# Kernel tuning notes

Measured on AMD Instinct MI355X. Metric: run time of the kernel, lower is better.

Reference implementation:

```python
import jax, jax.numpy as jnp
import numpy as np
from jax import lax

K = 7          # neighborhood kernel size
NUM_HEADS = 4
EPS = 1e-5


def layernorm(x, w, b):
    mu = x.mean(-1, keepdims=True)
    var = ((x - mu) ** 2).mean(-1, keepdims=True)
    return (x - mu) * lax.rsqrt(var + EPS) * w + b


def window_idx(n, k):
    # NATTEN border behavior: window is shifted (not shrunk) at edges.
    start = jnp.clip(jnp.arange(n) - k // 2, 0, n - k)
    return start[:, None] + jnp.arange(k)  # [n, k]


def neighborhood_attention(x, qkv_w, qkv_b, rpb, proj_w, proj_b):
    B, H, W, C = x.shape
    nh, k = NUM_HEADS, K
    hd = C // nh
    scale = hd ** -0.5
    qkv = (x @ qkv_w + qkv_b).reshape(B, H, W, 3, nh, hd)
    q = jnp.transpose(qkv[:, :, :, 0], (0, 3, 1, 2, 4)) * scale  # [B,nh,H,W,hd]
    kk = jnp.transpose(qkv[:, :, :, 1], (0, 3, 1, 2, 4))
    vv = jnp.transpose(qkv[:, :, :, 2], (0, 3, 1, 2, 4))

    ri = window_idx(H, k)  # [H,k]
    ci = window_idx(W, k)  # [W,k]

    def gather(t):  # [B,nh,H,W,hd] -> [B,nh,H,W,k,k,hd]
        t = t[:, :, ri]           # [B,nh,H,k,W,hd]
        t = t[:, :, :, :, ci]     # [B,nh,H,k,W,k,hd]
        return jnp.transpose(t, (0, 1, 2, 4, 3, 5, 6))

    k_nb = gather(kk)
    v_nb = gather(vv).reshape(B, nh, H, W, k * k, hd)

    attn = jnp.einsum('bnhwd,bnhwijd->bnhwij', q, k_nb)  # [B,nh,H,W,k,k]

    # relative positional bias, rpb: [nh, 2k-1, 2k-1]
    br = ri - jnp.arange(H)[:, None] + (k - 1)  # [H,k] in [0, 2k-2]
    bc = ci - jnp.arange(W)[:, None] + (k - 1)  # [W,k]
    bias = rpb[:, br]                 # [nh,H,k,2k-1]
    bias = bias[:, :, :, bc]          # [nh,H,k,W,k]
    bias = jnp.transpose(bias, (0, 1, 3, 2, 4))  # [nh,H,W,k,k]

    attn = jax.nn.softmax((attn + bias[None]).reshape(B, nh, H, W, k * k), axis=-1)
    out = jnp.einsum('bnhwl,bnhwld->bnhwd', attn, v_nb)
    out = jnp.transpose(out, (0, 2, 3, 1, 4)).reshape(B, H, W, C)
    return out @ proj_w + proj_b


def mlp(x, w1, b1, w2, b2):
    return jax.nn.gelu(x @ w1 + b1, approximate=False) @ w2 + b2


def nat_block_forward(x, norm1_w, norm1_b, qkv_w, qkv_b, rpb, proj_w, proj_b,
                      norm2_w, norm2_b, fc1_w, fc1_b, fc2_w, fc2_b,
                      conv_w, dnorm_w, dnorm_b):
    depth = norm1_w.shape[0]
    for i in range(depth):
        h = layernorm(x, norm1_w[i], norm1_b[i])
        h = neighborhood_attention(h, qkv_w[i], qkv_b[i], rpb[i], proj_w[i], proj_b[i])
        x = x + h
        x = x + mlp(layernorm(x, norm2_w[i], norm2_b[i]),
                    fc1_w[i], fc1_b[i], fc2_w[i], fc2_b[i])
    # ConvDownsampler: 3x3 stride-2 conv (no bias) + LayerNorm, channels-last
    y = lax.conv_general_dilated(x, conv_w, (2, 2), ((1, 1), (1, 1)),
                                 dimension_numbers=('NHWC', 'HWIO', 'NHWC'))
    y = layernorm(y, dnorm_w, dnorm_b)
    return (y, x)


def setup_inputs() -> dict:
    key = jax.random.key(0)
    ks = jax.random.split(key, 12)
    B, H, W, C = 2, 56, 56, 128
    depth, nh, k = 2, NUM_HEADS, K
    hidden = 4 * C
    init = lambda kk, shape: jax.random.normal(kk, shape, jnp.float32) * 0.02
    return {
        'x': jax.random.normal(ks[0], (B, H, W, C), jnp.float32),
        'norm1_w': jnp.ones((depth, C), jnp.float32),
        'norm1_b': jnp.zeros((depth, C), jnp.float32),
        'qkv_w': init(ks[1], (depth, C, 3 * C)),
        'qkv_b': jnp.zeros((depth, 3 * C), jnp.float32),
        'rpb': init(ks[2], (depth, nh, 2 * k - 1, 2 * k - 1)),
        'proj_w': init(ks[3], (depth, C, C)),
        'proj_b': jnp.zeros((depth, C), jnp.float32),
        'norm2_w': jnp.ones((depth, C), jnp.float32),
        'norm2_b': jnp.zeros((depth, C), jnp.float32),
        'fc1_w': init(ks[4], (depth, C, hidden)),
        'fc1_b': jnp.zeros((depth, hidden), jnp.float32),
        'fc2_w': init(ks[5], (depth, hidden, C)),
        'fc2_b': jnp.zeros((depth, C), jnp.float32),
        'conv_w': init(ks[6], (3, 3, C, 2 * C)),
        'dnorm_w': jnp.ones((2 * C,), jnp.float32),
        'dnorm_b': jnp.zeros((2 * C,), jnp.float32),
    }


def reference(x, norm1_w, norm1_b, qkv_w, qkv_b, rpb, proj_w, proj_b,
              norm2_w, norm2_b, fc1_w, fc1_b, fc2_w, fc2_b,
              conv_w, dnorm_w, dnorm_b):
    return nat_block_forward(x, norm1_w, norm1_b, qkv_w, qkv_b, rpb, proj_w,
                             proj_b, norm2_w, norm2_b, fc1_w, fc1_b, fc2_w,
                             fc2_b, conv_w, dnorm_w, dnorm_b)
```

## Files before the change

### kernel.cpp

```cpp
#include <hip/hip_runtime.h>
#include <stdint.h>


typedef __attribute__((ext_vector_type(8))) short bf16x8;
typedef __attribute__((ext_vector_type(4))) float f32x4;

__device__ __forceinline__ float bf2f(uint16_t u) {
  union { uint32_t u; float f; } t;
  t.u = (uint32_t)u << 16;
  return t.f;
}
__device__ __forceinline__ uint16_t f2bf(float f) {
  union { float f; uint32_t u; } t;
  t.f = f;
  return (uint16_t)((t.u + 0x7FFFu + ((t.u >> 16) & 1u)) >> 16);
}

struct PrepArgs {
  const float* src[9];
  uint16_t* dst[9];
  int K[9], N[9];
  int cum[10];
};

__global__ __launch_bounds__(256) void prep_weights(PrepArgs a) {
  __shared__ float t[32][33];
  int bt = blockIdx.x;
  int j = 0;
#pragma unroll
  for (int u = 0; u < 9; ++u)
    if (bt >= a.cum[u + 1]) j = u + 1;
  int lt = bt - a.cum[j];
  const float* w = a.src[j];
  uint16_t* wt = a.dst[j];
  int K = a.K[j], N = a.N[j];
  int tn = N >> 5;
  int n0 = (lt % tn) * 32, k0 = (lt / tn) * 32;
  int tx = threadIdx.x & 31, ty = threadIdx.x >> 5;
#pragma unroll
  for (int r2 = 0; r2 < 32; r2 += 8)
    t[ty + r2][tx] = w[(size_t)(k0 + ty + r2) * N + n0 + tx];
  __syncthreads();
#pragma unroll
  for (int r2 = 0; r2 < 32; r2 += 8)
    wt[(size_t)(n0 + ty + r2) * K + k0 + tx] = f2bf(t[tx][ty + r2]);
}

__global__ __launch_bounds__(256) void ln256_kernel(const float* __restrict__ p0,
                                                    const float* __restrict__ p1,
                                                    const float* __restrict__ p2,
                                                    float* __restrict__ out,
                                                    const float* __restrict__ w,
                                                    const float* __restrict__ b) {
  int wave = threadIdx.x >> 6, lane = threadIdx.x & 63;
  int pix = blockIdx.x * 4 + wave;
  size_t base = (size_t)pix * 256 + lane * 4;
  float4 a0 = *(const float4*)(p0 + base);
  float4 a1 = *(const float4*)(p1 + base);
  float4 a2 = *(const float4*)(p2 + base);
  float4 v;
  v.x = a0.x + a1.x + a2.x;
  v.y = a0.y + a1.y + a2.y;
  v.z = a0.z + a1.z + a2.z;
  v.w = a0.w + a1.w + a2.w;
  float s = v.x + v.y + v.z + v.w;
  float s2 = v.x * v.x + v.y * v.y + v.z * v.z + v.w * v.w;
#pragma unroll
  for (int off = 32; off; off >>= 1) {
    s += __shfl_xor(s, off, 64);
    s2 += __shfl_xor(s2, off, 64);
  }
  float mu = s * (1.f / 256.f);
  float var = s2 * (1.f / 256.f) - mu * mu;
  float r = rsqrtf(var + 1e-5f);
  float4 wv = *(const float4*)(w + lane * 4);
  float4 bv = *(const float4*)(b + lane * 4);
  float4 o;
  o.x = (v.x - mu) * r * wv.x + bv.x;
  o.y = (v.y - mu) * r * wv.y + bv.y;
  o.z = (v.z - mu) * r * wv.z + bv.z;
  o.w = (v.w - mu) * r * wv.w + bv.w;
  *(float4*)(out + base) = o;
}

template <int KD, int ND, int ACT, int RES, int OUTB, int LNF>
__global__ __launch_bounds__(256) void mfma_gemm32(
    const uint16_t* __restrict__ A, const float* __restrict__ Af,
    const float* __restrict__ lnw, const float* __restrict__ lnb,
    const uint16_t* __restrict__ Wt, const float* __restrict__ bias,
    const float* __restrict__ res, float* __restrict__ outf,
    uint16_t* __restrict__ outb, float* __restrict__ outf2, int M) {
  __shared__ __align__(16) char smem[26112];
  uint16_t(*sA)[136] = (uint16_t(*)[136])smem;
  uint16_t(*sB)[136] = (uint16_t(*)[136])(smem + 8704);
  float(*sC)[68] = (float(*)[68])smem;

  int m0 = blockIdx.x * 32, n0 = blockIdx.y * 64;
  int tid = threadIdx.x, lane = tid & 63, wid = tid >> 6;
  int wr = (wid >> 1) * 16, wc = (wid & 1) * 32;
  int lc = lane & 15, g = lane >> 4;
  int lko = g * 8;

  f32x4 acc0 = {0.f, 0.f, 0.f, 0.f}, acc1 = acc0;

  constexpr int NCH = KD / 128;
#pragma unroll
  for (int c = 0; c < NCH; ++c) {
    if constexpr (LNF) {
      int r = tid >> 3, qt = tid & 7;
      const float4* xr = (const float4*)(Af + (size_t)(m0 + r) * 128 + qt * 16);
      float4 xv[4];
      float s = 0.f, s2 = 0.f;
#pragma unroll
      for (int u = 0; u < 4; ++u) {
        xv[u] = xr[u];
        s += xv[u].x + xv[u].y + xv[u].z + xv[u].w;
        s2 += xv[u].x * xv[u].x + xv[u].y * xv[u].y + xv[u].z * xv[u].z + xv[u].w * xv[u].w;
      }
      s += __shfl_xor(s, 1, 64);
      s += __shfl_xor(s, 2, 64);
      s += __shfl_xor(s, 4, 64);
      s2 += __shfl_xor(s2, 1, 64);
      s2 += __shfl_xor(s2, 2, 64);
      s2 += __shfl_xor(s2, 4, 64);
      float mu = s * (1.f / 128.f);
      float var = s2 * (1.f / 128.f) - mu * mu;
      float rstd = rsqrtf(var + 1e-5f);
      const float* lw = lnw + qt * 16;
      const float* lb = lnb + qt * 16;
      union { uint16_t us[8]; bf16x8 v; } tq[2];
#pragma unroll
      for (int u = 0; u < 4; ++u) {
        tq[u >> 1].us[(u & 1) * 4 + 0] = f2bf((xv[u].x - mu) * rstd * lw[u * 4 + 0] + lb[u * 4 + 0]);
        tq[u >> 1].us[(u & 1) * 4 + 1] = f2bf((xv[u].y - mu) * rstd * lw[u * 4 + 1] + lb[u * 4 + 1]);
        tq[u >> 1].us[(u & 1) * 4 + 2] = f2bf((xv[u].z - mu) * rstd * lw[u * 4 + 2] + lb[u * 4 + 2]);
        tq[u >> 1].us[(u & 1) * 4 + 3] = f2bf((xv[u].w - mu) * rstd * lw[u * 4 + 3] + lb[u * 4 + 3]);
      }
      *(bf16x8*)&sA[r][qt * 16] = tq[0].v;
      *(bf16x8*)&sA[r][qt * 16 + 8] = tq[1].v;
    } else {
#pragma unroll
      for (int it = 0; it < 2; ++it) {
        int chunk = tid + it * 256;
        int row = chunk >> 4, kc = (chunk & 15) * 8;
        *(bf16x8*)&sA[row][kc] =
            *(const bf16x8*)(A + (size_t)(m0 + row) * KD + c * 128 + kc);
      }
    }
#pragma unroll
    for (int it = 0; it < 4; ++it) {
      int chunk = tid + it * 256;
      int row = chunk >> 4, kc = (chunk & 15) * 8;
      *(bf16x8*)&sB[row][kc] =
          *(const bf16x8*)(Wt + (size_t)(n0 + row) * KD + c * 128 + kc);
    }
    __syncthreads();
#pragma unroll
    for (int kk = 0; kk < 128; kk += 32) {
      bf16x8 a0 = *(const bf16x8*)&sA[wr + lc][kk + lko];
      bf16x8 b0 = *(const bf16x8*)&sB[wc + lc][kk + lko];
      bf16x8 b1 = *(const bf16x8*)&sB[wc + 16 + lc][kk + lko];
      acc0 = __builtin_amdgcn_mfma_f32_16x16x32_bf16(a0, b0, acc0, 0, 0, 0);
      acc1 = __builtin_amdgcn_mfma_f32_16x16x32_bf16(a0, b1, acc1, 0, 0, 0);
    }
    __syncthreads();
  }

  {
    float bv0 = bias ? bias[n0 + wc + lc] : 0.f;
    float bv1 = bias ? bias[n0 + wc + lc + 16] : 0.f;
#pragma unroll
    for (int ni = 0; ni < 2; ++ni) {
      float bv = ni ? bv1 : bv0;
      f32x4 av = ni ? acc1 : acc0;
#pragma unroll
      for (int j = 0; j < 4; ++j) {
        float a = av[j] + bv;
        if (ACT) a = 0.5f * a * (1.f + erff(a * 0.70710678118654752f));
        sC[wr + g * 4 + j][wc + ni * 16 + lc] = a;
      }
    }
    __syncthreads();
    int r = tid >> 3, cs = (tid & 7) * 8;
    int grow = m0 + r;
    if (grow < M) {
      const float4* cp = (const float4*)&sC[r][cs];
      float4 c4[2] = {cp[0], cp[1]};
      if (RES) {
        const float4* rp = (const float4*)(res + (size_t)grow * ND + n0 + cs);
#pragma unroll
        for (int u = 0; u < 2; ++u) {
          float4 rv = rp[u];
          c4[u].x += rv.x; c4[u].y += rv.y; c4[u].z += rv.z; c4[u].w += rv.w;
        }
      }
      if (OUTB) {
        union { uint16_t us[8]; bf16x8 v; } t;
#pragma unroll
        for (int u = 0; u < 2; ++u) {
          t.us[u * 4 + 0] = f2bf(c4[u].x);
          t.us[u * 4 + 1] = f2bf(c4[u].y);
          t.us[u * 4 + 2] = f2bf(c4[u].z);
          t.us[u * 4 + 3] = f2bf(c4[u].w);
        }
        *(bf16x8*)(outb + (size_t)grow * ND + n0 + cs) = t.v;
      } else {
        float4* op = (float4*)(outf + (size_t)grow * ND + n0 + cs);
        op[0] = c4[0];
        op[1] = c4[1];
        if (outf2) {
          float4* op2 = (float4*)(outf2 + (size_t)grow * ND + n0 + cs);
          op2[0] = c4[0];
          op2[1] = c4[1];
        }
      }
    }
  }
}

template <int KD, int ND>
__global__ __launch_bounds__(128) void mfma_gemm_s(
    const uint16_t* __restrict__ A, const uint16_t* __restrict__ Wt,
    const float* __restrict__ bias, const float* __restrict__ res,
    float* __restrict__ outf, float* __restrict__ outf2, int M) {
  __shared__ __align__(16) char smem[17408];
  uint16_t(*sA)[136] = (uint16_t(*)[136])smem;
  uint16_t(*sB)[136] = (uint16_t(*)[136])(smem + 8704);
  float(*sC)[36] = (float(*)[36])smem;

  int m0 = blockIdx.x * 32, n0 = blockIdx.y * 32;
  int tid = threadIdx.x, lane = tid & 63, wid = tid >> 6;
  int wr = wid * 16;
  int lc = lane & 15, g = lane >> 4;
  int lko = g * 8;

  f32x4 acc0 = {0.f, 0.f, 0.f, 0.f}, acc1 = acc0;

  constexpr int NCH = KD / 128;
#pragma unroll
  for (int c = 0; c < NCH; ++c) {
#pragma unroll
    for (int it = 0; it < 4; ++it) {
      int chunk = tid + it * 128;
      int row = chunk >> 4, kc = (chunk & 15) * 8;
      *(bf16x8*)&sA[row][kc] =
          *(const bf16x8*)(A + (size_t)(m0 + row) * KD + c * 128 + kc);
      *(bf16x8*)&sB[row][kc] =
          *(const bf16x8*)(Wt + (size_t)(n0 + row) * KD + c * 128 + kc);
    }
    __syncthreads();
#pragma unroll
    for (int kk = 0; kk < 128; kk += 32) {
      bf16x8 a0 = *(const bf16x8*)&sA[wr + lc][kk + lko];
      bf16x8 b0 = *(const bf16x8*)&sB[lc][kk + lko];
      bf16x8 b1 = *(const bf16x8*)&sB[16 + lc][kk + lko];
      acc0 = __builtin_amdgcn_mfma_f32_16x16x32_bf16(a0, b0, acc0, 0, 0, 0);
      acc1 = __builtin_amdgcn_mfma_f32_16x16x32_bf16(a0, b1, acc1, 0, 0, 0);
    }
    __syncthreads();
  }

  {
    float bv0 = bias[n0 + lc];
    float bv1 = bias[n0 + 16 + lc];
#pragma unroll
    for (int ni = 0; ni < 2; ++ni) {
      float bv = ni ? bv1 : bv0;
      f32x4 av = ni ? acc1 : acc0;
#pragma unroll
      for (int j = 0; j < 4; ++j)
        sC[wr + g * 4 + j][ni * 16 + lc] = av[j] + bv;
    }
    __syncthreads();
    int r = tid >> 2, cs = (tid & 3) * 8;
    int grow = m0 + r;
    if (grow < M) {
      const float4* cp = (const float4*)&sC[r][cs];
      float4 c4[2] = {cp[0], cp[1]};
      const float4* rp = (const float4*)(res + (size_t)grow * ND + n0 + cs);
#pragma unroll
      for (int u = 0; u < 2; ++u) {
        float4 rv = rp[u];
        c4[u].x += rv.x; c4[u].y += rv.y; c4[u].z += rv.z; c4[u].w += rv.w;
      }
      float4* op = (float4*)(outf + (size_t)grow * ND + n0 + cs);
      op[0] = c4[0];
      op[1] = c4[1];
      if (outf2) {
        float4* op2 = (float4*)(outf2 + (size_t)grow * ND + n0 + cs);
        op2[0] = c4[0];
        op2[1] = c4[1];
      }
    }
  }
}

#define KSWZ(row, colbytes) (((row) * 64 + (colbytes)) ^ (((row) & 7) << 4))

__global__ __launch_bounds__(128) void natten_mfma(const uint16_t* __restrict__ qkv,
                                                   const float* __restrict__ rpb,
                                                   uint16_t* __restrict__ out) {
  __shared__ uint16_t s_k[144 * 32];
  __shared__ uint16_t s_vt[32][168];
  __shared__ uint16_t s_p[32][168];
  __shared__ float s_rpb[169];

  int tid = threadIdx.x;
  int blk = blockIdx.x;
  int bh = blk & 7, tile = blk >> 3;
  int b = bh >> 2, head = bh & 3;
  int ti = tile / 7, tj = tile % 7;
  int i0 = ti * 4, j0 = tj * 8;
  int rbase = min(max(i0 - 3, 0), 46);
  int cbase = min(max(j0 - 3, 0), 42);

  const bf16x8 bz = {0, 0, 0, 0, 0, 0, 0, 0};
  const f32x4 fz = {0.f, 0.f, 0.f, 0.f};

  if (tid < 16)
    *(bf16x8*)((char*)s_k + KSWZ(140 + (tid >> 2), (tid & 3) * 16)) = bz;
  for (int idx = tid; idx < 640; idx += 128) s_vt[idx & 31][140 + (idx >> 5)] = 0;
  for (int idx = tid; idx < 512; idx += 128) s_p[idx & 31][144 + (idx >> 5)] = 0;
  for (int idx = tid; idx < 560; idx += 128) {
    int pos = idx >> 2, ch = (idx & 3) * 8;
    int r = rbase + pos / 14, c = cbase + pos % 14;
    const uint16_t* base = qkv + ((size_t)(b * 3136 + r * 56 + c)) * 384 + head * 32 + ch;
    bf16x8 kv = *(const bf16x8*)(base + 128);
    bf16x8 vv = *(const bf16x8*)(base + 256);
    *(bf16x8*)((char*)s_k + KSWZ(pos, ch * 2)) = kv;
#pragma unroll
    for (int e = 0; e < 8; ++e) s_vt[ch + e][pos] = (uint16_t)vv[e];
  }
  for (int idx = tid; idx < 169; idx += 128) s_rpb[idx] = rpb[head * 169 + idx];
  __syncthreads();

  int lane = tid & 63, wq = tid >> 6;
  int lc = lane & 15, g = lane >> 4;
  int q0 = wq * 16;

  int pA = q0 + lc;
  int piA = i0 + (pA >> 3), pjA = j0 + (pA & 7);
  bf16x8 qfrag =
      *(const bf16x8*)(qkv + ((size_t)(b * 3136 + piA * 56 + pjA)) * 384 + head * 32 + g * 8);

  f32x4 S[9];
#pragma unroll
  for (int t = 0; t < 9; ++t) {
    bf16x8 kfrag = *(const bf16x8*)((char*)s_k + KSWZ(t * 16 + lc, g * 16));
    S[t] = __builtin_amdgcn_mfma_f32_16x16x32_bf16(qfrag, kfrag, fz, 0, 0, 0);
  }

  int qi = wq * 2 + (g >> 1);
  int i = i0 + qi;
  int a = min(max(i - 3, 0), 49) - rbase;
  int brc = 6 - (i0 - rbase) - qi;
  int bj[4], bcc[4];
#pragma unroll
  for (int jj = 0; jj < 4; ++jj) {
    int qj = 4 * (g & 1) + jj;
    int j = j0 + qj;
    bj[jj] = min(max(j - 3, 0), 49) - cbase;
    bcc[jj] = 6 - (j0 - cbase) - qj;
  }

  float mx[4] = {-1e30f, -1e30f, -1e30f, -1e30f};
  int kr = (lc >= 14) ? 1 : 0;
  int kc = lc - 14 * kr;
#pragma unroll
  for (int t = 0; t < 9; ++t) {
    bool vr = (kr >= a) && (kr <= a + 6);
    int brrow = (kr + brc) * 13;
#pragma unroll
    for (int jj = 0; jj < 4; ++jj) {
      float sv = S[t][jj] * 0.17677669529663687f;
      bool v = vr && (kc >= bj[jj]) && (kc <= bj[jj] + 6);
      int bidx = v ? (brrow + kc + bcc[jj]) : 0;
      float val = v ? (sv + s_rpb[bidx]) : -1e30f;
      S[t][jj] = val;
      mx[jj] = fmaxf(mx[jj], val);
    }
    kr += 1;
    kc += 2;
    if (kc >= 14) { kc -= 14; kr += 1; }
  }
#pragma unroll
  for (int jj = 0; jj < 4; ++jj) {
#pragma unroll
    for (int off = 1; off < 16; off <<= 1) mx[jj] = fmaxf(mx[jj], __shfl_xor(mx[jj], off, 64));
  }

  float sm[4] = {0.f, 0.f, 0.f, 0.f};
#pragma unroll
  for (int t = 0; t < 9; ++t) {
#pragma unroll
    for (int jj = 0; jj < 4; ++jj) {
      float e = __expf(S[t][jj] - mx[jj]);
      sm[jj] += e;
      s_p[q0 + g * 4 + jj][t * 16 + lc] = f2bf(e);
    }
  }
#pragma unroll
  for (int jj = 0; jj < 4; ++jj) {
#pragma unroll
    for (int off = 1; off < 16; off <<= 1) sm[jj] += __shfl_xor(sm[jj], off, 64);
    sm[jj] = 1.f / sm[jj];
  }

  __syncthreads();

  f32x4 O[2] = {fz, fz};
#pragma unroll
  for (int ks = 0; ks < 5; ++ks) {
    bf16x8 pa = *(const bf16x8*)&s_p[q0 + lc][ks * 32 + g * 8];
#pragma unroll
    for (int dt = 0; dt < 2; ++dt) {
      bf16x8 vb = *(const bf16x8*)&s_vt[dt * 16 + lc][ks * 32 + g * 8];
      O[dt] = __builtin_amdgcn_mfma_f32_16x16x32_bf16(pa, vb, O[dt], 0, 0, 0);
    }
  }

#pragma unroll
  for (int jj = 0; jj < 4; ++jj) {
    int q = q0 + g * 4 + jj;
    int pi = i0 + (q >> 3), pj = j0 + (q & 7);
    size_t ob = ((size_t)(b * 3136 + pi * 56 + pj)) * 128 + head * 32;
    out[ob + lc] = f2bf(O[0][jj] * sm[jj]);
    out[ob + 16 + lc] = f2bf(O[1][jj] * sm[jj]);
  }
}

__global__ __launch_bounds__(256) void conv_gemm32(const float* __restrict__ x,
                                                   const uint16_t* __restrict__ Wt,
                                                   float* __restrict__ parts) {
  __shared__ __align__(16) char smem[26112];
  uint16_t(*sA)[136] = (uint16_t(*)[136])smem;
  uint16_t(*sB)[136] = (uint16_t(*)[136])(smem + 8704);
  float(*sC)[68] = (float(*)[68])smem;

  int m0 = blockIdx.x * 32, n0 = blockIdx.y * 64, kh = blockIdx.z;
  float* part = parts + (size_t)kh * 1568 * 256;
  int tid = threadIdx.x, lane = tid & 63, wid = tid >> 6;
  int wr = (wid >> 1) * 16, wc = (wid & 1) * 32;
  int lc = lane & 15, g = lane >> 4;
  int lko = g * 8;

  f32x4 acc0 = {0.f, 0.f, 0.f, 0.f}, acc1 = acc0;

  int r = tid >> 3, qt = tid & 7;
  int opix = m0 + r;
  int ow = opix % 28, oh = (opix / 28) % 28, bb = opix / 784;
  int ih = 2 * oh - 1 + kh;
  bool rowok = (ih >= 0) && (ih < 56);

#pragma unroll
  for (int kwc = 0; kwc < 3; ++kwc) {
    int iw = 2 * ow - 1 + kwc;
    float4 xv[4] = {{0.f, 0.f, 0.f, 0.f}, {0.f, 0.f, 0.f, 0.f},
                    {0.f, 0.f, 0.f, 0.f}, {0.f, 0.f, 0.f, 0.f}};
    if (rowok && iw >= 0 && iw < 56) {
      const float4* p =
          (const float4*)(x + (size_t)((bb * 56 + ih) * 56 + iw) * 128 + qt * 16);
#pragma unroll
      for (int u = 0; u < 4; ++u) xv[u] = p[u];
    }
    union { uint16_t us[8]; bf16x8 v; } tq[2];
#pragma unroll
    for (int u = 0; u < 4; ++u) {
      tq[u >> 1].us[(u & 1) * 4 + 0] = f2bf(xv[u].x);
      tq[u >> 1].us[(u & 1) * 4 + 1] = f2bf(xv[u].y);
      tq[u >> 1].us[(u & 1) * 4 + 2] = f2bf(xv[u].z);
      tq[u >> 1].us[(u & 1) * 4 + 3] = f2bf(xv[u].w);
    }
    *(bf16x8*)&sA[r][qt * 16] = tq[0].v;
    *(bf16x8*)&sA[r][qt * 16 + 8] = tq[1].v;
#pragma unroll
    for (int it = 0; it < 4; ++it) {
      int chunk = tid + it * 256;
      int row = chunk >> 4, kc = (chunk & 15) * 8;
      *(bf16x8*)&sB[row][kc] =
          *(const bf16x8*)(Wt + (size_t)(n0 + row) * 1152 + kh * 384 + kwc * 128 + kc);
    }
    __syncthreads();
#pragma unroll
    for (int kk = 0; kk < 128; kk += 32) {
      bf16x8 a0 = *(const bf16x8*)&sA[wr + lc][kk + lko];
      bf16x8 b0 = *(const bf16x8*)&sB[wc + lc][kk + lko];
      bf16x8 b1 = *(const bf16x8*)&sB[wc + 16 + lc][kk + lko];
      acc0 = __builtin_amdgcn_mfma_f32_16x16x32_bf16(a0, b0, acc0, 0, 0, 0);
      acc1 = __builtin_amdgcn_mfma_f32_16x16x32_bf16(a0, b1, acc1, 0, 0, 0);
    }
    __syncthreads();
  }

#pragma unroll
  for (int ni = 0; ni < 2; ++ni) {
    f32x4 av = ni ? acc1 : acc0;
#pragma unroll
    for (int j = 0; j < 4; ++j) sC[wr + g * 4 + j][wc + ni * 16 + lc] = av[j];
  }
  __syncthreads();
  int rr = tid >> 3, cs = (tid & 7) * 8;
  int grow = m0 + rr;
  if (grow < 1568) {
    const float4* cp = (const float4*)&sC[rr][cs];
    float4* op = (float4*)(part + (size_t)grow * 256 + n0 + cs);
    op[0] = cp[0];
    op[1] = cp[1];
  }
}

extern "C" void kernel_launch(void* const* d_in, const int* in_sizes, int n_in,
                              void* d_out, int out_size, void* d_ws, size_t ws_size,
                              hipStream_t stream) {
  const float* x    = (const float*)d_in[0];
  const float* n1w  = (const float*)d_in[1];
  const float* n1b  = (const float*)d_in[2];
  const float* qkvw = (const float*)d_in[3];
  const float* qkvb = (const float*)d_in[4];
  const float* rpb  = (const float*)d_in[5];
  const float* pw   = (const float*)d_in[6];
  const float* pb   = (const float*)d_in[7];
  const float* n2w  = (const float*)d_in[8];
  const float* n2b  = (const float*)d_in[9];
  const float* f1w  = (const float*)d_in[10];
  const float* f1b  = (const float*)d_in[11];
  const float* f2w  = (const float*)d_in[12];
  const float* f2b  = (const float*)d_in[13];
  const float* cw   = (const float*)d_in[14];
  const float* dnw  = (const float*)d_in[15];
  const float* dnb  = (const float*)d_in[16];
  float* out = (float*)d_out;

  char* wsb = (char*)d_ws;
  float*    xbuf    = (float*)(wsb + 0);
  uint16_t* qkv_b   = (uint16_t*)(wsb + 3211264);
  uint16_t* att_b   = (uint16_t*)(wsb + 8028160);
  uint16_t* hid_b   = (uint16_t*)(wsb + 9633792);
  float*    parts   = (float*)(wsb + 16056320);
  uint16_t* wts     = (uint16_t*)(wsb + 20873216);
  uint16_t* qkvwt = wts;
  uint16_t* pwt   = wts + 98304;
  uint16_t* f1wt  = wts + 131072;
  uint16_t* f2wt  = wts + 262144;
  uint16_t* cwt   = wts + 393216;

  PrepArgs pa;
  pa.src[0] = qkvw;         pa.dst[0] = qkvwt;          pa.K[0] = 128; pa.N[0] = 384;
  pa.src[1] = qkvw + 49152; pa.dst[1] = qkvwt + 49152;  pa.K[1] = 128; pa.N[1] = 384;
  pa.src[2] = pw;           pa.dst[2] = pwt;            pa.K[2] = 128; pa.N[2] = 128;
  pa.src[3] = pw + 16384;   pa.dst[3] = pwt + 16384;    pa.K[3] = 128; pa.N[3] = 128;
  pa.src[4] = f1w;          pa.dst[4] = f1wt;           pa.K[4] = 128; pa.N[4] = 512;
  pa.src[5] = f1w + 65536;  pa.dst[5] = f1wt + 65536;   pa.K[5] = 128; pa.N[5] = 512;
  pa.src[6] = f2w;          pa.dst[6] = f2wt;           pa.K[6] = 512; pa.N[6] = 128;
  pa.src[7] = f2w + 65536;  pa.dst[7] = f2wt + 65536;   pa.K[7] = 512; pa.N[7] = 128;
  pa.src[8] = cw;           pa.dst[8] = cwt;            pa.K[8] = 1152; pa.N[8] = 256;
  int cums[10] = {0, 48, 96, 112, 128, 192, 256, 320, 384, 672};
  for (int u = 0; u < 10; ++u) pa.cum[u] = cums[u];
  prep_weights<<<672, 256, 0, stream>>>(pa);

  for (int i = 0; i < 2; ++i) {
    const float* xin = (i == 0) ? x : xbuf;
    mfma_gemm32<128, 384, 0, 0, 1, 1><<<dim3(196, 6), 256, 0, stream>>>(
        nullptr, xin, n1w + i * 128, n1b + i * 128, qkvwt + i * 49152, qkvb + i * 384,
        nullptr, nullptr, qkv_b, nullptr, 6272);
    natten_mfma<<<784, 128, 0, stream>>>(qkv_b, rpb + i * 676, att_b);
    mfma_gemm_s<128, 128><<<dim3(196, 4), 128, 0, stream>>>(
        att_b, pwt + i * 16384, pb + i * 128, xin, xbuf, nullptr, 6272);
    mfma_gemm32<128, 512, 1, 0, 1, 1><<<dim3(196, 8), 256, 0, stream>>>(
        nullptr, xbuf, n2w + i * 128, n2b + i * 128, f1wt + i * 65536, f1b + i * 512,
        nullptr, nullptr, hid_b, nullptr, 6272);
    mfma_gemm_s<512, 128><<<dim3(196, 4), 128, 0, stream>>>(
        hid_b, f2wt + i * 65536, f2b + i * 128, xbuf, xbuf,
        (i == 1) ? (out + 401408) : nullptr, 6272);
  }

  conv_gemm32<<<dim3(49, 4, 3), 256, 0, stream>>>(xbuf, cwt, parts);
  ln256_kernel<<<392, 256, 0, stream>>>(parts, parts + 401408, parts + 802816, out, dnw, dnb);
}
```

Before: 99.14 us.

## Fuse attention projection, LayerNorm, MLP fc1/GELU/fc2 and residuals into one kernel

Replaces three kernels per layer (proj GEMM with residual, LN+fc1+GELU GEMM, fc2 GEMM with residual) with one kernel that processes 16 rows per 512-thread block. The hidden activations stay in shared memory, so the bf16 hidden buffer and the intermediate fp32 x no longer make a round trip through global memory, and two launches per layer go away. In exchange, every block reloads the full weight matrices into LDS in 128-row chunks with syncs in between. Only 392 blocks are launched, so per-block serialization and weight reload traffic may limit throughput.

```diff
diff --git a/kernel.cpp b/kernel.cpp
--- a/kernel.cpp
+++ b/kernel.cpp
@@ -218,80 +218,149 @@
   }
 }
 
-template <int KD, int ND>
-__global__ __launch_bounds__(128) void mfma_gemm_s(
-    const uint16_t* __restrict__ A, const uint16_t* __restrict__ Wt,
-    const float* __restrict__ bias, const float* __restrict__ res,
-    float* __restrict__ outf, float* __restrict__ outf2, int M) {
-  __shared__ __align__(16) char smem[17408];
-  uint16_t(*sA)[136] = (uint16_t(*)[136])smem;
-  uint16_t(*sB)[136] = (uint16_t(*)[136])(smem + 8704);
-  float(*sC)[36] = (float(*)[36])smem;
-
-  int m0 = blockIdx.x * 32, n0 = blockIdx.y * 32;
-  int tid = threadIdx.x, lane = tid & 63, wid = tid >> 6;
-  int wr = wid * 16;
+__global__ __launch_bounds__(512) void mlp_fused2(
+    const uint16_t* __restrict__ att,
+    const float* __restrict__ xin,
+    const uint16_t* __restrict__ pwt,
+    const float* __restrict__ pb,
+    const float* __restrict__ n2w, const float* __restrict__ n2b,
+    const uint16_t* __restrict__ f1wt,
+    const float* __restrict__ f1b,
+    const uint16_t* __restrict__ f2wt,
+    const float* __restrict__ f2b,
+    float* __restrict__ xout,
+    float* __restrict__ out2) {
+  __shared__ __align__(16) uint16_t sW[128][136];
+  __shared__ __align__(16) uint16_t sA[16][136];
+  __shared__ __align__(16) float sY[16][132];
+  __shared__ __align__(16) char sHraw[16640];
+  uint16_t(*sH)[520] = (uint16_t(*)[520])sHraw;
+  float(*sC)[132] = (float(*)[132])sHraw;
+
+  const f32x4 fz = {0.f, 0.f, 0.f, 0.f};
+  int m0 = blockIdx.x * 16;
+  int tid = threadIdx.x;
+  int lane = tid & 63, wid = tid >> 6;
   int lc = lane & 15, g = lane >> 4;
-  int lko = g * 8;
-
-  f32x4 acc0 = {0.f, 0.f, 0.f, 0.f}, acc1 = acc0;
-
-  constexpr int NCH = KD / 128;
-#pragma unroll
-  for (int c = 0; c < NCH; ++c) {
+  int rr = tid >> 5, cc = tid & 31;
+
+  float4 rx = *(const float4*)(xin + (size_t)(m0 + rr) * 128 + cc * 4);
+
+  if (tid < 256) {
+    int r = tid >> 4, q = tid & 15;
+    *(bf16x8*)&sA[r][q * 8] = *(const bf16x8*)(att + (size_t)(m0 + r) * 128 + q * 8);
+  }
+#pragma unroll
+  for (int it = 0; it < 4; ++it) {
+    int chunk = tid + it * 512;
+    int row = chunk >> 4, q = chunk & 15;
+    *(bf16x8*)&sW[row][q * 8] = *(const bf16x8*)(pwt + (size_t)row * 128 + q * 8);
+  }
+  __syncthreads();
+
+  {
+    f32x4 acc = fz;
+#pragma unroll
+    for (int ks = 0; ks < 4; ++ks) {
+      bf16x8 a = *(const bf16x8*)&sA[lc][ks * 32 + g * 8];
+      bf16x8 b = *(const bf16x8*)&sW[wid * 16 + lc][ks * 32 + g * 8];
+      acc = __builtin_amdgcn_mfma_f32_16x16x32_bf16(a, b, acc, 0, 0, 0);
+    }
+    float bv = pb[wid * 16 + lc];
+#pragma unroll
+    for (int j = 0; j < 4; ++j) sY[g * 4 + j][wid * 16 + lc] = acc[j] + bv;
+  }
+  __syncthreads();
+
+  {
+    float4 sv = *(const float4*)&sY[rr][cc * 4];
+    float4 y;
+    y.x = sv.x + rx.x; y.y = sv.y + rx.y; y.z = sv.z + rx.z; y.w = sv.w + rx.w;
+    float s = y.x + y.y + y.z + y.w;
+    float s2 = y.x * y.x + y.y * y.y + y.z * y.z + y.w * y.w;
+#pragma unroll
+    for (int off = 1; off < 32; off <<= 1) {
+      s += __shfl_xor(s, off, 64);
+      s2 += __shfl_xor(s2, off, 64);
+    }
+    float mu = s * (1.f / 128.f);
+    float var = s2 * (1.f / 128.f) - mu * mu;
+    float rstd = rsqrtf(var + 1e-5f);
+    *(float4*)&sY[rr][cc * 4] = y;
+    float4 lw = *(const float4*)(n2w + cc * 4);
+    float4 lb = *(const float4*)(n2b + cc * 4);
+    ushort4 nv;
+    nv.x = f2bf((y.x - mu) * rstd * lw.x + lb.x);
+    nv.y = f2bf((y.y - mu) * rstd * lw.y + lb.y);
+    nv.z = f2bf((y.z - mu) * rstd * lw.z + lb.z);
+    nv.w = f2bf((y.w - mu) * rstd * lw.w + lb.w);
+    *(ushort4*)&sA[rr][cc * 4] = nv;
+  }
+  __syncthreads();
+
+#pragma unroll 1
+  for (int ch = 0; ch < 4; ++ch) {
 #pragma unroll
     for (int it = 0; it < 4; ++it) {
-      int chunk = tid + it * 128;
-      int row = chunk >> 4, kc = (chunk & 15) * 8;
-      *(bf16x8*)&sA[row][kc] =
-          *(const bf16x8*)(A + (size_t)(m0 + row) * KD + c * 128 + kc);
-      *(bf16x8*)&sB[row][kc] =
-          *(const bf16x8*)(Wt + (size_t)(n0 + row) * KD + c * 128 + kc);
-    }
-    __syncthreads();
-#pragma unroll
-    for (int kk = 0; kk < 128; kk += 32) {
-      bf16x8 a0 = *(const bf16x8*)&sA[wr + lc][kk + lko];
-      bf16x8 b0 = *(const bf16x8*)&sB[lc][kk + lko];
-      bf16x8 b1 = *(const bf16x8*)&sB[16 + lc][kk + lko];
-      acc0 = __builtin_amdgcn_mfma_f32_16x16x32_bf16(a0, b0, acc0, 0, 0, 0);
-      acc1 = __builtin_amdgcn_mfma_f32_16x16x32_bf16(a0, b1, acc1, 0, 0, 0);
+      int chunk = tid + it * 512;
+      int row = chunk >> 4, q = chunk & 15;
+      *(bf16x8*)&sW[row][q * 8] =
+          *(const bf16x8*)(f1wt + (size_t)(ch * 128 + row) * 128 + q * 8);
+    }
+    __syncthreads();
+    f32x4 acc = fz;
+#pragma unroll
+    for (int ks = 0; ks < 4; ++ks) {
+      bf16x8 a = *(const bf16x8*)&sA[lc][ks * 32 + g * 8];
+      bf16x8 b = *(const bf16x8*)&sW[wid * 16 + lc][ks * 32 + g * 8];
+      acc = __builtin_amdgcn_mfma_f32_16x16x32_bf16(a, b, acc, 0, 0, 0);
+    }
+    int col = ch * 128 + wid * 16 + lc;
+    float bv = f1b[col];
+#pragma unroll
+    for (int j = 0; j < 4; ++j) {
+      float h = acc[j] + bv;
+      h = 0.5f * h * (1.f + erff(h * 0.70710678118654752f));
+      sH[g * 4 + j][col] = f2bf(h);
+    }
+    __syncthreads();
+  }
+
+  f32x4 acc2 = fz;
+#pragma unroll 1
+  for (int ch = 0; ch < 4; ++ch) {
+#pragma unroll
+    for (int it = 0; it < 4; ++it) {
+      int chunk = tid + it * 512;
+      int row = chunk >> 4, q = chunk & 15;
+      *(bf16x8*)&sW[row][q * 8] =
+          *(const bf16x8*)(f2wt + (size_t)row * 512 + ch * 128 + q * 8);
+    }
+    __syncthreads();
+#pragma unroll
+    for (int ks = 0; ks < 4; ++ks) {
+      bf16x8 a = *(const bf16x8*)&sH[lc][ch * 128 + ks * 32 + g * 8];
+      bf16x8 b = *(const bf16x8*)&sW[wid * 16 + lc][ks * 32 + g * 8];
+      acc2 = __builtin_amdgcn_mfma_f32_16x16x32_bf16(a, b, acc2, 0, 0, 0);
     }
     __syncthreads();
   }
 
   {
-    float bv0 = bias[n0 + lc];
-    float bv1 = bias[n0 + 16 + lc];
-#pragma unroll
-    for (int ni = 0; ni < 2; ++ni) {
-      float bv = ni ? bv1 : bv0;
-      f32x4 av = ni ? acc1 : acc0;
-#pragma unroll
-      for (int j = 0; j < 4; ++j)
-        sC[wr + g * 4 + j][ni * 16 + lc] = av[j] + bv;
-    }
-    __syncthreads();
-    int r = tid >> 2, cs = (tid & 3) * 8;
-    int grow = m0 + r;
-    if (grow < M) {
-      const float4* cp = (const float4*)&sC[r][cs];
-      float4 c4[2] = {cp[0], cp[1]};
-      const float4* rp = (const float4*)(res + (size_t)grow * ND + n0 + cs);
-#pragma unroll
-      for (int u = 0; u < 2; ++u) {
-        float4 rv = rp[u];
-        c4[u].x += rv.x; c4[u].y += rv.y; c4[u].z += rv.z; c4[u].w += rv.w;
-      }
-      float4* op = (float4*)(outf + (size_t)grow * ND + n0 + cs);
-      op[0] = c4[0];
-      op[1] = c4[1];
-      if (outf2) {
-        float4* op2 = (float4*)(outf2 + (size_t)grow * ND + n0 + cs);
-        op2[0] = c4[0];
-        op2[1] = c4[1];
-      }
-    }
+    int col = wid * 16 + lc;
+    float bv = f2b[col];
+#pragma unroll
+    for (int j = 0; j < 4; ++j) sC[g * 4 + j][col] = acc2[j] + bv;
+  }
+  __syncthreads();
+
+  {
+    float4 cv = *(const float4*)&sC[rr][cc * 4];
+    float4 yv = *(const float4*)&sY[rr][cc * 4];
+    float4 o;
+    o.x = cv.x + yv.x; o.y = cv.y + yv.y; o.z = cv.z + yv.z; o.w = cv.w + yv.w;
+    *(float4*)(xout + (size_t)(m0 + rr) * 128 + cc * 4) = o;
+    if (out2) *(float4*)(out2 + (size_t)(m0 + rr) * 128 + cc * 4) = o;
   }
 }
 
@@ -535,7 +604,6 @@
   float*    xbuf    = (float*)(wsb + 0);
   uint16_t* qkv_b   = (uint16_t*)(wsb + 3211264);
   uint16_t* att_b   = (uint16_t*)(wsb + 8028160);
-  uint16_t* hid_b   = (uint16_t*)(wsb + 9633792);
   float*    parts   = (float*)(wsb + 16056320);
   uint16_t* wts     = (uint16_t*)(wsb + 20873216);
   uint16_t* qkvwt = wts;
@@ -564,14 +632,10 @@
         nullptr, xin, n1w + i * 128, n1b + i * 128, qkvwt + i * 49152, qkvb + i * 384,
         nullptr, nullptr, qkv_b, nullptr, 6272);
     natten_mfma<<<784, 128, 0, stream>>>(qkv_b, rpb + i * 676, att_b);
-    mfma_gemm_s<128, 128><<<dim3(196, 4), 128, 0, stream>>>(
-        att_b, pwt + i * 16384, pb + i * 128, xin, xbuf, nullptr, 6272);
-    mfma_gemm32<128, 512, 1, 0, 1, 1><<<dim3(196, 8), 256, 0, stream>>>(
-        nullptr, xbuf, n2w + i * 128, n2b + i * 128, f1wt + i * 65536, f1b + i * 512,
-        nullptr, nullptr, hid_b, nullptr, 6272);
-    mfma_gemm_s<512, 128><<<dim3(196, 4), 128, 0, stream>>>(
-        hid_b, f2wt + i * 65536, f2b + i * 128, xbuf, xbuf,
-        (i == 1) ? (out + 401408) : nullptr, 6272);
+    mlp_fused2<<<392, 512, 0, stream>>>(
+        att_b, xin, pwt + i * 16384, pb + i * 128, n2w + i * 128, n2b + i * 128,
+        f1wt + i * 65536, f1b + i * 512, f2wt + i * 65536, f2b + i * 128,
+        xbuf, (i == 1) ? (out + 401408) : nullptr);
   }
 
   conv_gemm32<<<dim3(49, 4, 3), 256, 0, stream>>>(xbuf, cwt, parts);
```

New measurement: 87.30 us. -11.9%, faster.
